# Performance work log

Measured on AMD Instinct MI355X. Metric: run time of the kernel, lower is better.

Reference implementation:

```python
import jax, jax.numpy as jnp
import numpy as np
import math

D_MODEL = 64
N_HEADS = 4
D_HEAD = D_MODEL // N_HEADS
SCALE = math.sqrt(D_HEAD)
B, NQ, NK = 32, 16384, 31


def setup_inputs() -> dict:
    key = jax.random.key(0)
    kq, kk, kv, km, kw, kb = jax.random.split(key, 6)
    Q = jax.random.normal(kq, (B, NQ, D_MODEL), dtype=jnp.float32)
    K = jax.random.normal(kk, (B, NK, D_MODEL), dtype=jnp.float32)
    V = jax.random.normal(kv, (B, NK, D_MODEL), dtype=jnp.float32)
    mask = jax.random.randint(km, (B, NK), 0, 2).astype(jnp.bool_)
    # out_proj: nn.Linear(d_model, d_model)
    lim = 1.0 / math.sqrt(D_MODEL)
    W_out = jax.random.uniform(kw, (D_MODEL, D_MODEL), minval=-lim, maxval=lim, dtype=jnp.float32)
    b_out = jax.random.uniform(kb, (D_MODEL,), minval=-lim, maxval=lim, dtype=jnp.float32)
    return {"Q": Q, "K": K, "V": V, "mask": mask, "W_out": W_out, "b_out": b_out}


def reference(Q, K, V, mask, W_out, b_out):
    Bn, Nq, D = Q.shape
    Nk = K.shape[1]
    # (B, H, N, d_head)
    q = Q.reshape(Bn, Nq, N_HEADS, D_HEAD).transpose(0, 2, 1, 3)
    k = K.reshape(Bn, Nk, N_HEADS, D_HEAD).transpose(0, 2, 1, 3)
    v = V.reshape(Bn, Nk, N_HEADS, D_HEAD).transpose(0, 2, 1, 3)
    # (B, H, Nq, Nk)
    attn = jnp.einsum('bhqd,bhkd->bhqk', q, k) / SCALE
    attn = jnp.where(mask[:, None, None, :], attn, -jnp.inf)
    attn = jax.nn.softmax(attn, axis=-1)
    attn = jnp.nan_to_num(attn, nan=0.0)
    out = jnp.einsum('bhqk,bhkd->bhqd', attn, v)
    out = out.transpose(0, 2, 1, 3).reshape(Bn, Nq, D)
    return out @ W_out.T + b_out
```

## Files before the change

### kernel.cpp

```cpp
#include <hip/hip_runtime.h>
#include <math.h>

typedef _Float16 half4_t __attribute__((ext_vector_type(4)));
typedef _Float16 half8_t __attribute__((ext_vector_type(8)));
typedef __fp16   fp16x2  __attribute__((ext_vector_type(2)));
typedef float    f32x4   __attribute__((ext_vector_type(4)));

#define B_   32
#define NQ_  16384
#define NK_  31
#define DM_  64
#define BLK_PER_B 64
#define ITERS 4
#define KSCALE 0.3606738222635048f

static __device__ __forceinline__ half4_t cvt4(f32x4 f) {
  fp16x2 lo = __builtin_amdgcn_cvt_pkrtz(f[0], f[1]);
  fp16x2 hi = __builtin_amdgcn_cvt_pkrtz(f[2], f[3]);
  half4_t r;
  r[0] = (_Float16)lo[0]; r[1] = (_Float16)lo[1];
  r[2] = (_Float16)hi[0]; r[3] = (_Float16)hi[1];
  return r;
}

__global__ __launch_bounds__(256) void attn(
    const float* __restrict__ Q, const float* __restrict__ K,
    const float* __restrict__ V, const unsigned char* __restrict__ mraw,
    const float* __restrict__ W, const float* __restrict__ bout,
    float* __restrict__ out) {
  int b    = blockIdx.x >> 6;
  int blk  = blockIdx.x & 63;
  int tid  = threadIdx.x;
  int wave = tid >> 6, lane = tid & 63;
  int lq = lane & 15, quad = lane >> 4;

  __shared__ half8_t lds_kf[4][64];
  __shared__ half8_t lds_vw[8][2][64];

  const f32x4 fzero = {0.f, 0.f, 0.f, 0.f};

  int w = blk * 4 + wave;
  const float* qrow = Q + ((size_t)b * NQ_ + lq) * DM_ + 4 * quad;

  f32x4 qbuf[ITERS][4];
  #pragma unroll
  for (int d = 0; d < ITERS; ++d)
    #pragma unroll
    for (int h = 0; h < 4; ++h)
      qbuf[d][h] =
          *(const f32x4*)(qrow + (size_t)((w + d * 256) * 16) * DM_ + 16 * h);
  __builtin_amdgcn_sched_barrier(0);

  unsigned mb;
  {
    unsigned char c0 = 0, c1 = 0;
    if (lane < 62) { c0 = mraw[2 * lane]; c1 = mraw[2 * lane + 1]; }
    unsigned long long m3f =
        __ballot(lane < 62 && (c0 == 0x3f || c1 == 0x3f));
    unsigned long long moff =
        __ballot(lane < 62 && ((((2 * lane) & 3) != 0 && c0 != 0) || c1 != 0));
    int mode = m3f ? 2 : (moff ? 0 : 1);
    int nz = 0;
    if (lane < NK_) {
      int idx = b * NK_ + lane;
      nz = (mode == 0) ? (mraw[idx] != 0)
         : (mode == 1) ? (((const int*)mraw)[idx] != 0)
                       : (((const float*)mraw)[idx] != 0.0f);
    }
    mb = (unsigned)__ballot(nz) & 0x7fffffffu;
  }

  f32x4 cbias[2];
  #pragma unroll
  for (int tt = 0; tt < 2; ++tt)
    #pragma unroll
    for (int r = 0; r < 4; ++r) {
      int key = 16 * tt + 4 * quad + r;
      cbias[tt][r] = ((mb >> key) & 1u) ? 0.0f : -1e30f;
    }

  #pragma unroll
  for (int j = 0; j < 2; ++j) {
    int f  = wave * 2 + j;
    int tt = f >> 2, h = f & 3;
    int k  = 16 * tt + lq;
    f32x4 fv = fzero;
    if (k < NK_)
      fv = *(const f32x4*)(K + ((size_t)b * NK_ + k) * DM_ + 16 * h + 4 * quad);
    ((half4_t*)&lds_kf[h][lane])[tt] = cvt4(fv * KSCALE);
  }

  {
    half4_t af[8];
    #pragma unroll
    for (int s = 0; s < 8; ++s) {
      int k = 16 * (s & 1) + lq, h = s >> 1;
      f32x4 f = fzero;
      if (k < NK_)
        f = *(const f32x4*)(V + ((size_t)b * NK_ + k) * DM_ + 16 * h + 4 * quad);
      af[s] = cvt4(f);
    }
    half4_t bf[4];
    #pragma unroll
    for (int h = 0; h < 4; ++h) {
      f32x4 f = *(const f32x4*)(W + (16 * wave + lq) * DM_ + 16 * h + 4 * quad);
      bf[h] = cvt4(f);
    }
    #pragma unroll
    for (int s = 0; s < 8; ++s) {
      f32x4 m = __builtin_amdgcn_mfma_f32_16x16x16f16(af[s], bf[s >> 1],
                                                      fzero, 0, 0, 0);
      ((half4_t*)&lds_vw[s][wave >> 1][lane])[wave & 1] = cvt4(m);
    }
  }

  f32x4 bias[4];
  #pragma unroll
  for (int dt = 0; dt < 4; ++dt)
    bias[dt] = *(const f32x4*)(bout + 16 * dt + 4 * quad);

  __syncthreads();

  #pragma unroll
  for (int it = 0; it < ITERS; ++it) {
    half4_t qf[4];
    #pragma unroll
    for (int h = 0; h < 4; ++h) qf[h] = cvt4(qbuf[it][h]);

    half4_t pf[8];
    #pragma unroll
    for (int h = 0; h < 4; ++h) {
      half8_t kk = lds_kf[h][lane];
      half4_t k0 = __builtin_shufflevector(kk, kk, 0, 1, 2, 3);
      half4_t k1 = __builtin_shufflevector(kk, kk, 4, 5, 6, 7);
      f32x4 c0 = __builtin_amdgcn_mfma_f32_16x16x16f16(k0, qf[h], cbias[0], 0, 0, 0);
      f32x4 c1 = __builtin_amdgcn_mfma_f32_16x16x16f16(k1, qf[h], cbias[1], 0, 0, 0);
      f32x4 e0, e1;
      #pragma unroll
      for (int r = 0; r < 4; ++r) {
        e0[r] = __builtin_amdgcn_exp2f(c0[r]);
        e1[r] = __builtin_amdgcn_exp2f(c1[r]);
      }
      float sum = (e0[0] + e0[1]) + (e0[2] + e0[3]) +
                  (e1[0] + e1[1]) + (e1[2] + e1[3]);
      sum += __shfl_xor(sum, 16);
      sum += __shfl_xor(sum, 32);
      float inv = (sum > 0.f) ? __builtin_amdgcn_rcpf(sum) : 0.f;
      pf[2 * h + 0] = cvt4(e0 * inv);
      pf[2 * h + 1] = cvt4(e1 * inv);
    }

    f32x4 acc[4] = {fzero, fzero, fzero, fzero};
    #pragma unroll
    for (int s = 0; s < 8; ++s) {
      half8_t v01 = lds_vw[s][0][lane];
      half8_t v23 = lds_vw[s][1][lane];
      half4_t a0 = __builtin_shufflevector(v01, v01, 0, 1, 2, 3);
      half4_t a1 = __builtin_shufflevector(v01, v01, 4, 5, 6, 7);
      half4_t a2 = __builtin_shufflevector(v23, v23, 0, 1, 2, 3);
      half4_t a3 = __builtin_shufflevector(v23, v23, 4, 5, 6, 7);
      acc[0] = __builtin_amdgcn_mfma_f32_16x16x16f16(a0, pf[s], acc[0], 0, 0, 0);
      acc[1] = __builtin_amdgcn_mfma_f32_16x16x16f16(a1, pf[s], acc[1], 0, 0, 0);
      acc[2] = __builtin_amdgcn_mfma_f32_16x16x16f16(a2, pf[s], acc[2], 0, 0, 0);
      acc[3] = __builtin_amdgcn_mfma_f32_16x16x16f16(a3, pf[s], acc[3], 0, 0, 0);
    }

    int q0 = (w + it * 256) * 16;
    float* obase = out + ((size_t)b * NQ_ + q0 + lq) * DM_ + 4 * quad;
    #pragma unroll
    for (int dt = 0; dt < 4; ++dt)
      *(f32x4*)(obase + 16 * dt) = acc[dt] + bias[dt];
  }
}

extern "C" void kernel_launch(void* const* d_in, const int* in_sizes, int n_in,
                              void* d_out, int out_size, void* d_ws, size_t ws_size,
                              hipStream_t stream) {
  const float*         Q    = (const float*)d_in[0];
  const float*         K    = (const float*)d_in[1];
  const float*         V    = (const float*)d_in[2];
  const unsigned char* mask = (const unsigned char*)d_in[3];
  const float*         W    = (const float*)d_in[4];
  const float*         bo   = (const float*)d_in[5];
  float*               out  = (float*)d_out;

  hipLaunchKernelGGL(attn, dim3(B_ * BLK_PER_B), dim3(256), 0, stream,
                     Q, K, V, mask, W, bo, out);
}
```

Baseline: 252.1 us.

## Stage Q loads and output stores through swizzled LDS for coalesced access

Q tiles are now loaded with fully contiguous per-wave 16-byte-per-lane reads and transposed into the MFMA fragment layout through a per-wave swizzled LDS buffer. Outputs are likewise written to LDS and re-read so each global store is contiguous. Prefetch depth drops from all four iterations up front to one iteration ahead, which cuts register pressure but exposes more load latency. It adds LDS traffic and relies on wave-local ordering with no explicit barrier.

```diff
diff --git a/kernel.cpp b/kernel.cpp
--- a/kernel.cpp
+++ b/kernel.cpp
@@ -36,20 +36,19 @@
 
   __shared__ half8_t lds_kf[4][64];
   __shared__ half8_t lds_vw[8][2][64];
+  __shared__ f32x4 stg[4][16][16];
 
   const f32x4 fzero = {0.f, 0.f, 0.f, 0.f};
 
   int w = blk * 4 + wave;
-  const float* qrow = Q + ((size_t)b * NQ_ + lq) * DM_ + 4 * quad;
-
-  f32x4 qbuf[ITERS][4];
-  #pragma unroll
-  for (int d = 0; d < ITERS; ++d)
-    #pragma unroll
-    for (int h = 0; h < 4; ++h)
-      qbuf[d][h] =
-          *(const f32x4*)(qrow + (size_t)((w + d * 256) * 16) * DM_ + 16 * h);
-  __builtin_amdgcn_sched_barrier(0);
+
+  f32x4 qst[4];
+  {
+    const float* qb0 = Q + ((size_t)b * NQ_ + (size_t)w * 16) * DM_;
+    #pragma unroll
+    for (int j = 0; j < 4; ++j)
+      qst[j] = *(const f32x4*)(qb0 + j * 256 + lane * 4);
+  }
 
   unsigned mb;
   {
@@ -123,9 +122,28 @@
 
   #pragma unroll
   for (int it = 0; it < ITERS; ++it) {
+    int q0 = (w + it * 256) * 16;
+
+    #pragma unroll
+    for (int j = 0; j < 4; ++j) {
+      int row = 4 * j + quad;
+      stg[wave][row][lq ^ (row & 7)] = qst[j];
+    }
+
+    if (it + 1 < ITERS) {
+      const float* nb =
+          Q + ((size_t)b * NQ_ + (size_t)(w + (it + 1) * 256) * 16) * DM_;
+      #pragma unroll
+      for (int j = 0; j < 4; ++j)
+        qst[j] = *(const f32x4*)(nb + j * 256 + lane * 4);
+    }
+
     half4_t qf[4];
     #pragma unroll
-    for (int h = 0; h < 4; ++h) qf[h] = cvt4(qbuf[it][h]);
+    for (int h = 0; h < 4; ++h) {
+      f32x4 qv = stg[wave][lq][(4 * h + quad) ^ (lq & 7)];
+      qf[h] = cvt4(qv);
+    }
 
     half4_t pf[8];
     #pragma unroll
@@ -165,11 +183,17 @@
       acc[3] = __builtin_amdgcn_mfma_f32_16x16x16f16(a3, pf[s], acc[3], 0, 0, 0);
     }
 
-    int q0 = (w + it * 256) * 16;
-    float* obase = out + ((size_t)b * NQ_ + q0 + lq) * DM_ + 4 * quad;
     #pragma unroll
     for (int dt = 0; dt < 4; ++dt)
-      *(f32x4*)(obase + 16 * dt) = acc[dt] + bias[dt];
+      stg[wave][lq][(4 * dt + quad) ^ (lq & 7)] = acc[dt] + bias[dt];
+
+    float* ob = out + ((size_t)b * NQ_ + q0) * DM_;
+    #pragma unroll
+    for (int j = 0; j < 4; ++j) {
+      int row = 4 * j + quad;
+      f32x4 ov = stg[wave][row][lq ^ (row & 7)];
+      *(f32x4*)(ob + j * 256 + lane * 4) = ov;
+    }
   }
 }
 
```

Result: no change. 247.9 us (-1.7%).

## Stream Q tiles into LDS via async DMA with double buffering and coalesced stores

Applied to the files above, without the earlier changes.

Q tiles are no longer prefetched into registers up front. Each wave now issues global_load_lds DMA into a double-buffered, XOR-swizzled LDS tile and overlaps the next tile's load with compute using manual vmcnt waits. Output goes through the same LDS buffer so each row is written as contiguous 16-byte chunks. K fragments are kept in registers instead of LDS, and the bias is folded into the accumulator init. The aim is lower register pressure, better occupancy and more coalesced writes, at the cost of extra LDS traffic and fragile hand-written waitcnt ordering.

```diff
diff --git a/kernel.cpp b/kernel.cpp
--- a/kernel.cpp
+++ b/kernel.cpp
@@ -13,6 +13,9 @@
 #define BLK_PER_B 64
 #define ITERS 4
 #define KSCALE 0.3606738222635048f
+
+#define AS1 __attribute__((address_space(1)))
+#define AS3 __attribute__((address_space(3)))
 
 static __device__ __forceinline__ half4_t cvt4(f32x4 f) {
   fp16x2 lo = __builtin_amdgcn_cvt_pkrtz(f[0], f[1]);
@@ -34,22 +37,27 @@
   int wave = tid >> 6, lane = tid & 63;
   int lq = lane & 15, quad = lane >> 4;
 
-  __shared__ half8_t lds_kf[4][64];
   __shared__ half8_t lds_vw[8][2][64];
+  __shared__ f32x4 lds_q[4][2][16][16];
 
   const f32x4 fzero = {0.f, 0.f, 0.f, 0.f};
-
   int w = blk * 4 + wave;
-  const float* qrow = Q + ((size_t)b * NQ_ + lq) * DM_ + 4 * quad;
-
-  f32x4 qbuf[ITERS][4];
-  #pragma unroll
-  for (int d = 0; d < ITERS; ++d)
-    #pragma unroll
-    for (int h = 0; h < 4; ++h)
-      qbuf[d][h] =
-          *(const f32x4*)(qrow + (size_t)((w + d * 256) * 16) * DM_ + 16 * h);
-  __builtin_amdgcn_sched_barrier(0);
+  const float* qbatch = Q + (size_t)b * NQ_ * DM_;
+
+  auto dma_tile = [&](int it, int buf) {
+    const float* qt = qbatch + (size_t)(w + it * 256) * 16 * DM_;
+    #pragma unroll
+    for (int j = 0; j < 4; ++j) {
+      int row = 4 * j + quad;
+      const float* src = qt + row * DM_ + ((lq ^ (row & 7)) << 2);
+      __builtin_amdgcn_global_load_lds(
+          (const AS1 void*)(const void*)src,
+          (AS3 void*)(void*)((char*)&lds_q[wave][buf][0][0] + j * 1024),
+          16, 0, 0);
+    }
+  };
+
+  dma_tile(0, 0);
 
   unsigned mb;
   {
@@ -79,15 +87,17 @@
       cbias[tt][r] = ((mb >> key) & 1u) ? 0.0f : -1e30f;
     }
 
-  #pragma unroll
-  for (int j = 0; j < 2; ++j) {
-    int f  = wave * 2 + j;
-    int tt = f >> 2, h = f & 3;
-    int k  = 16 * tt + lq;
-    f32x4 fv = fzero;
-    if (k < NK_)
-      fv = *(const f32x4*)(K + ((size_t)b * NK_ + k) * DM_ + 16 * h + 4 * quad);
-    ((half4_t*)&lds_kf[h][lane])[tt] = cvt4(fv * KSCALE);
+  half4_t kf[2][4];
+  #pragma unroll
+  for (int tt = 0; tt < 2; ++tt) {
+    int k = 16 * tt + lq;
+    #pragma unroll
+    for (int h = 0; h < 4; ++h) {
+      f32x4 f = fzero;
+      if (k < NK_)
+        f = *(const f32x4*)(K + ((size_t)b * NK_ + k) * DM_ + 16 * h + 4 * quad);
+      kf[tt][h] = cvt4(f * KSCALE);
+    }
   }
 
   {
@@ -122,19 +132,27 @@
   __syncthreads();
 
   #pragma unroll
-  for (int it = 0; it < ITERS; ++it) {
+  for (int t = 0; t < ITERS; ++t) {
+    const int buf = t & 1;
+
+    if (t + 1 < ITERS) dma_tile(t + 1, buf ^ 1);
+
+    if (t == 0 || t + 1 == ITERS)
+      asm volatile("s_waitcnt vmcnt(4)" ::: "memory");
+    else
+      asm volatile("s_waitcnt vmcnt(8)" ::: "memory");
+    __builtin_amdgcn_sched_barrier(0);
+
     half4_t qf[4];
     #pragma unroll
-    for (int h = 0; h < 4; ++h) qf[h] = cvt4(qbuf[it][h]);
+    for (int h = 0; h < 4; ++h)
+      qf[h] = cvt4(lds_q[wave][buf][lq][(4 * h + quad) ^ (lq & 7)]);
 
     half4_t pf[8];
     #pragma unroll
     for (int h = 0; h < 4; ++h) {
-      half8_t kk = lds_kf[h][lane];
-      half4_t k0 = __builtin_shufflevector(kk, kk, 0, 1, 2, 3);
-      half4_t k1 = __builtin_shufflevector(kk, kk, 4, 5, 6, 7);
-      f32x4 c0 = __builtin_amdgcn_mfma_f32_16x16x16f16(k0, qf[h], cbias[0], 0, 0, 0);
-      f32x4 c1 = __builtin_amdgcn_mfma_f32_16x16x16f16(k1, qf[h], cbias[1], 0, 0, 0);
+      f32x4 c0 = __builtin_amdgcn_mfma_f32_16x16x16f16(kf[0][h], qf[h], cbias[0], 0, 0, 0);
+      f32x4 c1 = __builtin_amdgcn_mfma_f32_16x16x16f16(kf[1][h], qf[h], cbias[1], 0, 0, 0);
       f32x4 e0, e1;
       #pragma unroll
       for (int r = 0; r < 4; ++r) {
@@ -150,7 +168,7 @@
       pf[2 * h + 1] = cvt4(e1 * inv);
     }
 
-    f32x4 acc[4] = {fzero, fzero, fzero, fzero};
+    f32x4 acc[4] = {bias[0], bias[1], bias[2], bias[3]};
     #pragma unroll
     for (int s = 0; s < 8; ++s) {
       half8_t v01 = lds_vw[s][0][lane];
@@ -165,11 +183,17 @@
       acc[3] = __builtin_amdgcn_mfma_f32_16x16x16f16(a3, pf[s], acc[3], 0, 0, 0);
     }
 
-    int q0 = (w + it * 256) * 16;
-    float* obase = out + ((size_t)b * NQ_ + q0 + lq) * DM_ + 4 * quad;
     #pragma unroll
     for (int dt = 0; dt < 4; ++dt)
-      *(f32x4*)(obase + 16 * dt) = acc[dt] + bias[dt];
+      lds_q[wave][buf][lq][(4 * dt + quad) ^ (lq & 7)] = acc[dt];
+
+    float* ot = out + ((size_t)b * NQ_ + (size_t)(w + t * 256) * 16) * DM_;
+    #pragma unroll
+    for (int j = 0; j < 4; ++j) {
+      int row = 4 * j + quad;
+      f32x4 ov = lds_q[wave][buf][row][lq ^ (row & 7)];
+      *(f32x4*)(ot + row * DM_ + lq * 4) = ov;
+    }
   }
 }
 
```

Result: no change. 247.4 us (-1.9%).
